# Kernel optimization log

Measured on AMD Instinct MI355X. Metric: run time of the kernel, lower is better.

Reference implementation:

```python
import jax, jax.numpy as jnp
import numpy as np

SEQ = 4096
D = 1024


def setup_inputs() -> dict:
    key = jax.random.key(0)
    kx, kq, kk, kv = jax.random.split(key, 4)
    x = jax.random.normal(kx, (SEQ, D), dtype=jnp.float32)
    W_Q = jax.random.normal(kq, (D, D), dtype=jnp.float32)
    W_K = jax.random.normal(kk, (D, D), dtype=jnp.float32)
    W_V = jax.random.normal(kv, (D, D), dtype=jnp.float32)
    b_Q = jnp.zeros((D,), dtype=jnp.float32)
    b_K = jnp.zeros((D,), dtype=jnp.float32)
    b_V = jnp.zeros((D,), dtype=jnp.float32)
    return {"x": x, "W_Q": W_Q, "W_K": W_K, "W_V": W_V,
            "b_Q": b_Q, "b_K": b_K, "b_V": b_V}


def reference(x, W_Q, W_K, W_V, b_Q, b_K, b_V):
    d_head = W_Q.shape[0]
    q = x @ W_Q + b_Q                      # [S, D]
    k = x @ W_K + b_K                      # [S, D]
    v = x @ W_V + b_V                      # [S, D]
    scores = (q @ k.T) / jnp.sqrt(jnp.float32(d_head))  # [S, S]
    probs = jax.nn.softmax(scores, axis=-1)              # softmax over last axis
    return probs @ v                        # [S, D]
```

## Files before the change

kernel.cpp:

```cpp
#include <hip/hip_runtime.h>
#include <hip/hip_bf16.h>
#include <stdint.h>

#define SEQLEN 4096
#define DMODEL 1024

typedef uint16_t u16;
typedef uint32_t u32;

typedef __bf16 bf16x8 __attribute__((ext_vector_type(8)));
typedef float  f32x4  __attribute__((ext_vector_type(4)));
typedef u16    u16x8  __attribute__((ext_vector_type(8)));
typedef u16    u16x4  __attribute__((ext_vector_type(4)));

__device__ __forceinline__ u16 f2bf(float f) {
  union { float f; u32 u; } a; a.f = f;
  return (u16)((a.u + 0x7FFFu + ((a.u >> 16) & 1u)) >> 16);
}
__device__ __forceinline__ float bf2f(u16 h) {
  union { u32 u; float f; } a; a.u = ((u32)h) << 16;
  return a.f;
}

__device__ __forceinline__ void gl_lds16(const u16* g, u16* l) {
  __builtin_amdgcn_global_load_lds(
      (const __attribute__((address_space(1))) void*)g,
      (__attribute__((address_space(3))) void*)l,
      16, 0, 0);
}

__device__ __forceinline__ void stage_tile(const u16* __restrict__ g, int ld,
                                           int row0, int k0, u16* lds, int tid) {
#pragma unroll
  for (int it = 0; it < 4; ++it) {
    int u = tid + 256 * it;
    int row = u >> 3;
    int cg = (u & 7) ^ (row & 7);
    gl_lds16(g + (size_t)(row0 + row) * ld + (size_t)(k0 + cg * 8), lds + u * 8);
  }
}

__device__ __forceinline__ bf16x8 ld_frag(const u16* lds, int row, int chunk) {
  return *(const bf16x8*)(lds + row * 64 + ((chunk ^ (row & 7)) << 3));
}

#define MFMA16(c, a, b) c = __builtin_amdgcn_mfma_f32_16x16x32_bf16(a, b, c, 0, 0, 0)

__global__ void split_x_kernel(const float* __restrict__ x,
                               u16* __restrict__ xh, u16* __restrict__ xl) {
  const int total = SEQLEN * DMODEL / 4;
  for (int idx = blockIdx.x * 256 + threadIdx.x; idx < total; idx += gridDim.x * 256) {
    float4 f = ((const float4*)x)[idx];
    float ff[4] = {f.x, f.y, f.z, f.w};
    union { u16x4 v; u16 s[4]; } h, l;
#pragma unroll
    for (int uu = 0; uu < 4; ++uu) {
      u16 hi = f2bf(ff[uu]);
      h.s[uu] = hi;
      l.s[uu] = f2bf(ff[uu] - bf2f(hi));
    }
    ((u16x4*)xh)[idx] = h.v;
    ((u16x4*)xl)[idx] = l.v;
  }
}

__global__ void transpose_w_kernel(const float* __restrict__ W,
                                   u16* __restrict__ wth, u16* __restrict__ wtl) {
  __shared__ float tile[64][65];
  int n0 = (blockIdx.x & 15) * 64;
  int k0 = (blockIdx.x >> 4) * 64;
  int c = threadIdx.x & 63, r0 = threadIdx.x >> 6;
#pragma unroll
  for (int rr = 0; rr < 16; ++rr) {
    int r = r0 * 16 + rr;
    tile[r][c] = W[(size_t)(k0 + r) * DMODEL + n0 + c];
  }
  __syncthreads();
#pragma unroll
  for (int rr = 0; rr < 16; ++rr) {
    int n = r0 * 16 + rr;
    float f = tile[c][n];
    u16 hi = f2bf(f);
    wth[(size_t)(n0 + n) * DMODEL + k0 + c] = hi;
    wtl[(size_t)(n0 + n) * DMODEL + k0 + c] = f2bf(f - bf2f(hi));
  }
}

template <bool THREE, bool SPLITOUT>
__global__ __launch_bounds__(256, 2) void proj_kernel(
    const u16* __restrict__ Ah, const u16* __restrict__ Al,
    const u16* __restrict__ Bh, const u16* __restrict__ Bl,
    const float* __restrict__ bias, float scale,
    u16* __restrict__ outh, u16* __restrict__ outl, u16* __restrict__ outT) {
  __shared__ __align__(16) u16 sAh[128 * 64];
  __shared__ __align__(16) u16 sBh[128 * 64];
  __shared__ __align__(16) u16 sAl[THREE ? 128 * 64 : 8];
  __shared__ __align__(16) u16 sBl[THREE ? 128 * 64 : 8];

  int tid = threadIdx.x;
  int lane = tid & 63, wid = tid >> 6;
  int wr = (wid >> 1) * 64, wc = (wid & 1) * 64;
  int r = lane & 15, g = lane >> 4;
  int m0 = blockIdx.x * 128, n0 = blockIdx.y * 128;

  f32x4 acc[4][4];
#pragma unroll
  for (int i = 0; i < 4; ++i)
#pragma unroll
    for (int j = 0; j < 4; ++j) acc[i][j] = (f32x4){0.f, 0.f, 0.f, 0.f};

  for (int step = 0; step < DMODEL / 64; ++step) {
    int k0 = step * 64;
    __syncthreads();
    stage_tile(Ah, DMODEL, m0, k0, sAh, tid);
    stage_tile(Bh, DMODEL, n0, k0, sBh, tid);
    if (THREE) {
      stage_tile(Al, DMODEL, m0, k0, sAl, tid);
      stage_tile(Bl, DMODEL, n0, k0, sBl, tid);
    }
    __syncthreads();
#pragma unroll
    for (int ks = 0; ks < 2; ++ks) {
      bf16x8 fa[4], fb[4], fal[4], fbl[4];
#pragma unroll
      for (int i = 0; i < 4; ++i) {
        fa[i] = ld_frag(sAh, wr + i * 16 + r, ks * 4 + g);
        fb[i] = ld_frag(sBh, wc + i * 16 + r, ks * 4 + g);
      }
      if (THREE) {
#pragma unroll
        for (int i = 0; i < 4; ++i) {
          fal[i] = ld_frag(sAl, wr + i * 16 + r, ks * 4 + g);
          fbl[i] = ld_frag(sBl, wc + i * 16 + r, ks * 4 + g);
        }
      }
#pragma unroll
      for (int i = 0; i < 4; ++i)
#pragma unroll
        for (int j = 0; j < 4; ++j) {
          MFMA16(acc[i][j], fa[i], fb[j]);
          if (THREE) {
            MFMA16(acc[i][j], fa[i], fbl[j]);
            MFMA16(acc[i][j], fal[i], fb[j]);
          }
        }
    }
  }
#pragma unroll
  for (int i = 0; i < 4; ++i)
#pragma unroll
    for (int j = 0; j < 4; ++j) {
      int col = n0 + wc + j * 16 + r;
      float bv = bias[col];
#pragma unroll
      for (int t = 0; t < 4; ++t) {
        int row = m0 + wr + i * 16 + g * 4 + t;
        float v = (acc[i][j][t] + bv) * scale;
        if (SPLITOUT) {
          u16 hi = f2bf(v);
          outh[(size_t)row * DMODEL + col] = hi;
          outl[(size_t)row * DMODEL + col] = f2bf(v - bf2f(hi));
        } else {
          outT[(size_t)col * SEQLEN + row] = f2bf(v);
        }
      }
    }
}

__global__ __launch_bounds__(256, 2) void scores_kernel(
    const u16* __restrict__ qh, const u16* __restrict__ ql,
    const u16* __restrict__ kh, const u16* __restrict__ kl,
    u16* __restrict__ P, float* __restrict__ mloc, float* __restrict__ tsum) {
  __shared__ __align__(16) float sS[128 * 129];
  u16* sAh = (u16*)sS;
  u16* sAl = sAh + 128 * 64;
  u16* sBh = sAl + 128 * 64;
  u16* sBl = sBh + 128 * 64;

  int tid = threadIdx.x;
  int lane = tid & 63, wid = tid >> 6;
  int wr = (wid >> 1) * 64, wc = (wid & 1) * 64;
  int r = lane & 15, g = lane >> 4;
  int m0 = blockIdx.x * 128, n0 = blockIdx.y * 128;

  f32x4 acc[4][4];
#pragma unroll
  for (int i = 0; i < 4; ++i)
#pragma unroll
    for (int j = 0; j < 4; ++j) acc[i][j] = (f32x4){0.f, 0.f, 0.f, 0.f};

  for (int step = 0; step < DMODEL / 64; ++step) {
    int k0 = step * 64;
    __syncthreads();
    stage_tile(qh, DMODEL, m0, k0, sAh, tid);
    stage_tile(kh, DMODEL, n0, k0, sBh, tid);
    stage_tile(ql, DMODEL, m0, k0, sAl, tid);
    stage_tile(kl, DMODEL, n0, k0, sBl, tid);
    __syncthreads();
#pragma unroll
    for (int ks = 0; ks < 2; ++ks) {
      bf16x8 fa[4], fb[4], fal[4], fbl[4];
#pragma unroll
      for (int i = 0; i < 4; ++i) {
        fa[i] = ld_frag(sAh, wr + i * 16 + r, ks * 4 + g);
        fb[i] = ld_frag(sBh, wc + i * 16 + r, ks * 4 + g);
        fal[i] = ld_frag(sAl, wr + i * 16 + r, ks * 4 + g);
        fbl[i] = ld_frag(sBl, wc + i * 16 + r, ks * 4 + g);
      }
#pragma unroll
      for (int i = 0; i < 4; ++i)
#pragma unroll
        for (int j = 0; j < 4; ++j) {
          MFMA16(acc[i][j], fa[i], fb[j]);
          MFMA16(acc[i][j], fa[i], fbl[j]);
          MFMA16(acc[i][j], fal[i], fb[j]);
        }
    }
  }
  __syncthreads();
#pragma unroll
  for (int i = 0; i < 4; ++i)
#pragma unroll
    for (int j = 0; j < 4; ++j)
#pragma unroll
      for (int t = 0; t < 4; ++t)
        sS[(wr + i * 16 + g * 4 + t) * 129 + wc + j * 16 + r] = acc[i][j][t];
  __syncthreads();

  int rt = tid >> 1, h = tid & 1;
  const float* rowp = sS + rt * 129 + h * 64;
  float mx = -3.0e38f;
#pragma unroll 16
  for (int c = 0; c < 64; ++c) mx = fmaxf(mx, rowp[c]);
  mx = fmaxf(mx, __shfl_xor(mx, 1));

  float ssum = 0.f;
  int grow = m0 + rt;
  u16* pout = P + (size_t)grow * SEQLEN + n0 + h * 64;
#pragma unroll
  for (int c8 = 0; c8 < 8; ++c8) {
    union { u16 s[8]; u16x8 v; } tmp;
#pragma unroll
    for (int uu = 0; uu < 8; ++uu) {
      float e = exp2f((rowp[c8 * 8 + uu] - mx) * 1.4426950408889634f);
      ssum += e;
      tmp.s[uu] = f2bf(e);
    }
    *(u16x8*)(pout + c8 * 8) = tmp.v;
  }
  ssum += __shfl_xor(ssum, 1);
  if (h == 0) {
    mloc[(size_t)blockIdx.y * SEQLEN + grow] = mx;
    tsum[(size_t)blockIdx.y * SEQLEN + grow] = ssum;
  }
}

__global__ void finalize_kernel(const float* __restrict__ mloc,
                                const float* __restrict__ tsum,
                                float* __restrict__ rowscale) {
  int rr = blockIdx.x * 256 + threadIdx.x;
  if (rr >= SEQLEN) return;
  float M = -3.0e38f;
#pragma unroll
  for (int t = 0; t < 32; ++t) M = fmaxf(M, mloc[t * SEQLEN + rr]);
  float l = 0.f;
#pragma unroll
  for (int t = 0; t < 32; ++t)
    l += tsum[t * SEQLEN + rr] * exp2f((mloc[t * SEQLEN + rr] - M) * 1.4426950408889634f);
  float inv = 1.0f / l;
#pragma unroll
  for (int t = 0; t < 32; ++t)
    rowscale[t * SEQLEN + rr] = exp2f((mloc[t * SEQLEN + rr] - M) * 1.4426950408889634f) * inv;
}

__global__ void pnorm_kernel(u16* __restrict__ P, const float* __restrict__ rowscale) {
  const int total = SEQLEN * SEQLEN / 8;
  for (int idx = blockIdx.x * 256 + threadIdx.x; idx < total; idx += gridDim.x * 256) {
    int rrow = idx >> 9;
    int c8 = idx & 511;
    int t = c8 >> 4;
    float sc = rowscale[t * SEQLEN + rrow];
    union { u16x8 v; u16 s[8]; } d;
    d.v = ((u16x8*)P)[idx];
#pragma unroll
    for (int uu = 0; uu < 8; ++uu) d.s[uu] = f2bf(bf2f(d.s[uu]) * sc);
    ((u16x8*)P)[idx] = d.v;
  }
}

__global__ __launch_bounds__(256, 2) void pv_kernel(const u16* __restrict__ P,
                                                    const u16* __restrict__ vT,
                                                    float* __restrict__ out) {
  __shared__ __align__(16) u16 sA[128 * 64];
  __shared__ __align__(16) u16 sB[128 * 64];
  int tid = threadIdx.x;
  int lane = tid & 63, wid = tid >> 6;
  int wr = (wid >> 1) * 64, wc = (wid & 1) * 64;
  int r = lane & 15, g = lane >> 4;
  int m0 = blockIdx.x * 128, n0 = blockIdx.y * 128;

  f32x4 acc[4][4];
#pragma unroll
  for (int i = 0; i < 4; ++i)
#pragma unroll
    for (int j = 0; j < 4; ++j) acc[i][j] = (f32x4){0.f, 0.f, 0.f, 0.f};

  for (int step = 0; step < SEQLEN / 64; ++step) {
    int k0 = step * 64;
    __syncthreads();
    stage_tile(P, SEQLEN, m0, k0, sA, tid);
    stage_tile(vT, SEQLEN, n0, k0, sB, tid);
    __syncthreads();
#pragma unroll
    for (int ks = 0; ks < 2; ++ks) {
      bf16x8 fa[4], fb[4];
#pragma unroll
      for (int i = 0; i < 4; ++i) {
        fa[i] = ld_frag(sA, wr + i * 16 + r, ks * 4 + g);
        fb[i] = ld_frag(sB, wc + i * 16 + r, ks * 4 + g);
      }
#pragma unroll
      for (int i = 0; i < 4; ++i)
#pragma unroll
        for (int j = 0; j < 4; ++j) MFMA16(acc[i][j], fa[i], fb[j]);
    }
  }
#pragma unroll
  for (int i = 0; i < 4; ++i)
#pragma unroll
    for (int j = 0; j < 4; ++j)
#pragma unroll
      for (int t = 0; t < 4; ++t)
        out[(size_t)(m0 + wr + i * 16 + g * 4 + t) * DMODEL + n0 + wc + j * 16 + r] =
            acc[i][j][t];
}

extern "C" void kernel_launch(void* const* d_in, const int* in_sizes, int n_in,
                              void* d_out, int out_size, void* d_ws, size_t ws_size,
                              hipStream_t stream) {
  (void)in_sizes; (void)n_in; (void)out_size; (void)ws_size;
  const float* x  = (const float*)d_in[0];
  const float* WQ = (const float*)d_in[1];
  const float* WK = (const float*)d_in[2];
  const float* WV = (const float*)d_in[3];
  const float* bQ = (const float*)d_in[4];
  const float* bK = (const float*)d_in[5];
  const float* bV = (const float*)d_in[6];
  float* out = (float*)d_out;
  char* ws = (char*)d_ws;
  const size_t MB = 1ull << 20;

  u16* xh   = (u16*)(ws + 0);
  u16* xl   = (u16*)(ws + 8 * MB);
  u16* wqh  = (u16*)(ws + 16 * MB);
  u16* wql  = (u16*)(ws + 18 * MB);
  u16* wkh  = (u16*)(ws + 20 * MB);
  u16* wkl  = (u16*)(ws + 22 * MB);
  u16* wvh  = (u16*)(ws + 24 * MB);
  u16* wvl  = (u16*)(ws + 26 * MB);
  u16* P    = (u16*)(ws + 0);
  u16* qh   = (u16*)(ws + 32 * MB);
  u16* ql   = (u16*)(ws + 40 * MB);
  u16* kh   = (u16*)(ws + 48 * MB);
  u16* kl   = (u16*)(ws + 56 * MB);
  u16* vT   = (u16*)(ws + 64 * MB);
  float* mloc     = (float*)(ws + 72 * MB);
  float* tsum     = (float*)(ws + 72 * MB + 512 * 1024);
  float* rowscale = (float*)(ws + 73 * MB);

  split_x_kernel<<<2048, 256, 0, stream>>>(x, xh, xl);
  transpose_w_kernel<<<256, 256, 0, stream>>>(WQ, wqh, wql);
  transpose_w_kernel<<<256, 256, 0, stream>>>(WK, wkh, wkl);
  transpose_w_kernel<<<256, 256, 0, stream>>>(WV, wvh, wvl);

  dim3 gproj(32, 8);
  proj_kernel<true, true><<<gproj, 256, 0, stream>>>(xh, xl, wqh, wql, bQ,
                                                     1.0f / 32.0f, qh, ql, nullptr);
  proj_kernel<true, true><<<gproj, 256, 0, stream>>>(xh, xl, wkh, wkl, bK,
                                                     1.0f, kh, kl, nullptr);
  proj_kernel<false, false><<<gproj, 256, 0, stream>>>(xh, nullptr, wvh, nullptr, bV,
                                                       1.0f, nullptr, nullptr, vT);

  dim3 gsc(32, 32);
  scores_kernel<<<gsc, 256, 0, stream>>>(qh, ql, kh, kl, P, mloc, tsum);
  finalize_kernel<<<16, 256, 0, stream>>>(mloc, tsum, rowscale);
  pnorm_kernel<<<4096, 256, 0, stream>>>(P, rowscale);

  dim3 gpv(32, 8);
  pv_kernel<<<gpv, 256, 0, stream>>>(P, vT, out);
}
```

Before: 341.4 us.

## Double-buffer LDS staging in projection, scores and PV GEMM kernels

Converts the GEMM main loops to a double-buffered LDS scheme. The next K-tile is prefetched with global_load_lds while the current tile feeds the MFMAs, so there is one barrier per step instead of two. The three-pass split-bf16 kernels halve the K-step to 32 with a new swizzle, keeping LDS at 64KB. This aims to hide global load latency behind compute. The costs are more LDS per block, which may limit occupancy, and a possible race because the async loads are not explicitly waited on before the barrier.

```diff
diff --git a/kernel.cpp b/kernel.cpp
--- a/kernel.cpp
+++ b/kernel.cpp
@@ -29,8 +29,8 @@
       16, 0, 0);
 }
 
-__device__ __forceinline__ void stage_tile(const u16* __restrict__ g, int ld,
-                                           int row0, int k0, u16* lds, int tid) {
+__device__ __forceinline__ void stage64(const u16* __restrict__ g, int ld,
+                                        int row0, int k0, u16* lds, int tid) {
 #pragma unroll
   for (int it = 0; it < 4; ++it) {
     int u = tid + 256 * it;
@@ -39,9 +39,21 @@
     gl_lds16(g + (size_t)(row0 + row) * ld + (size_t)(k0 + cg * 8), lds + u * 8);
   }
 }
-
-__device__ __forceinline__ bf16x8 ld_frag(const u16* lds, int row, int chunk) {
+__device__ __forceinline__ void stage32(const u16* __restrict__ g, int ld,
+                                        int row0, int k0, u16* lds, int tid) {
+#pragma unroll
+  for (int it = 0; it < 2; ++it) {
+    int u = tid + 256 * it;
+    int row = u >> 2;
+    int cg = (u & 3) ^ ((row >> 1) & 3);
+    gl_lds16(g + (size_t)(row0 + row) * ld + (size_t)(k0 + cg * 8), lds + u * 8);
+  }
+}
+__device__ __forceinline__ bf16x8 frag64(const u16* lds, int row, int chunk) {
   return *(const bf16x8*)(lds + row * 64 + ((chunk ^ (row & 7)) << 3));
+}
+__device__ __forceinline__ bf16x8 frag32(const u16* lds, int row, int chunk) {
+  return *(const bf16x8*)(lds + row * 32 + ((chunk ^ ((row >> 1) & 3)) << 3));
 }
 
 #define MFMA16(c, a, b) c = __builtin_amdgcn_mfma_f32_16x16x32_bf16(a, b, c, 0, 0, 0)
@@ -92,10 +104,7 @@
     const u16* __restrict__ Bh, const u16* __restrict__ Bl,
     const float* __restrict__ bias, float scale,
     u16* __restrict__ outh, u16* __restrict__ outl, u16* __restrict__ outT) {
-  __shared__ __align__(16) u16 sAh[128 * 64];
-  __shared__ __align__(16) u16 sBh[128 * 64];
-  __shared__ __align__(16) u16 sAl[THREE ? 128 * 64 : 8];
-  __shared__ __align__(16) u16 sBl[THREE ? 128 * 64 : 8];
+  __shared__ __align__(16) u16 st[32768];
 
   int tid = threadIdx.x;
   int lane = tid & 63, wid = tid >> 6;
@@ -109,43 +118,73 @@
 #pragma unroll
     for (int j = 0; j < 4; ++j) acc[i][j] = (f32x4){0.f, 0.f, 0.f, 0.f};
 
-  for (int step = 0; step < DMODEL / 64; ++step) {
-    int k0 = step * 64;
+  if (THREE) {
+    stage32(Ah, DMODEL, m0, 0, st + 0 * 4096, tid);
+    stage32(Al, DMODEL, m0, 0, st + 1 * 4096, tid);
+    stage32(Bh, DMODEL, n0, 0, st + 2 * 4096, tid);
+    stage32(Bl, DMODEL, n0, 0, st + 3 * 4096, tid);
     __syncthreads();
-    stage_tile(Ah, DMODEL, m0, k0, sAh, tid);
-    stage_tile(Bh, DMODEL, n0, k0, sBh, tid);
-    if (THREE) {
-      stage_tile(Al, DMODEL, m0, k0, sAl, tid);
-      stage_tile(Bl, DMODEL, n0, k0, sBl, tid);
-    }
-    __syncthreads();
-#pragma unroll
-    for (int ks = 0; ks < 2; ++ks) {
+    int c = 0;
+    for (int step = 0; step < DMODEL / 32; ++step) {
+      if (step + 1 < DMODEL / 32) {
+        int k0 = (step + 1) * 32;
+        u16* nb = st + (c ^ 1) * 16384;
+        stage32(Ah, DMODEL, m0, k0, nb + 0 * 4096, tid);
+        stage32(Al, DMODEL, m0, k0, nb + 1 * 4096, tid);
+        stage32(Bh, DMODEL, n0, k0, nb + 2 * 4096, tid);
+        stage32(Bl, DMODEL, n0, k0, nb + 3 * 4096, tid);
+      }
+      const u16* cb = st + c * 16384;
       bf16x8 fa[4], fb[4], fal[4], fbl[4];
 #pragma unroll
       for (int i = 0; i < 4; ++i) {
-        fa[i] = ld_frag(sAh, wr + i * 16 + r, ks * 4 + g);
-        fb[i] = ld_frag(sBh, wc + i * 16 + r, ks * 4 + g);
-      }
-      if (THREE) {
-#pragma unroll
-        for (int i = 0; i < 4; ++i) {
-          fal[i] = ld_frag(sAl, wr + i * 16 + r, ks * 4 + g);
-          fbl[i] = ld_frag(sBl, wc + i * 16 + r, ks * 4 + g);
-        }
+        fa[i]  = frag32(cb + 0 * 4096, wr + i * 16 + r, g);
+        fal[i] = frag32(cb + 1 * 4096, wr + i * 16 + r, g);
+        fb[i]  = frag32(cb + 2 * 4096, wc + i * 16 + r, g);
+        fbl[i] = frag32(cb + 3 * 4096, wc + i * 16 + r, g);
       }
 #pragma unroll
       for (int i = 0; i < 4; ++i)
 #pragma unroll
         for (int j = 0; j < 4; ++j) {
           MFMA16(acc[i][j], fa[i], fb[j]);
-          if (THREE) {
-            MFMA16(acc[i][j], fa[i], fbl[j]);
-            MFMA16(acc[i][j], fal[i], fb[j]);
-          }
+          MFMA16(acc[i][j], fa[i], fbl[j]);
+          MFMA16(acc[i][j], fal[i], fb[j]);
         }
-    }
-  }
+      __syncthreads();
+      c ^= 1;
+    }
+  } else {
+    stage64(Ah, DMODEL, m0, 0, st + 0 * 8192, tid);
+    stage64(Bh, DMODEL, n0, 0, st + 1 * 8192, tid);
+    __syncthreads();
+    int c = 0;
+    for (int step = 0; step < DMODEL / 64; ++step) {
+      if (step + 1 < DMODEL / 64) {
+        int k0 = (step + 1) * 64;
+        u16* nb = st + (c ^ 1) * 16384;
+        stage64(Ah, DMODEL, m0, k0, nb + 0 * 8192, tid);
+        stage64(Bh, DMODEL, n0, k0, nb + 1 * 8192, tid);
+      }
+      const u16* cb = st + c * 16384;
+#pragma unroll
+      for (int ks = 0; ks < 2; ++ks) {
+        bf16x8 fa[4], fb[4];
+#pragma unroll
+        for (int i = 0; i < 4; ++i) {
+          fa[i] = frag64(cb + 0 * 8192, wr + i * 16 + r, ks * 4 + g);
+          fb[i] = frag64(cb + 1 * 8192, wc + i * 16 + r, ks * 4 + g);
+        }
+#pragma unroll
+        for (int i = 0; i < 4; ++i)
+#pragma unroll
+          for (int j = 0; j < 4; ++j) MFMA16(acc[i][j], fa[i], fb[j]);
+      }
+      __syncthreads();
+      c ^= 1;
+    }
+  }
+
 #pragma unroll
   for (int i = 0; i < 4; ++i)
 #pragma unroll
@@ -171,11 +210,9 @@
     const u16* __restrict__ qh, const u16* __restrict__ ql,
     const u16* __restrict__ kh, const u16* __restrict__ kl,
     u16* __restrict__ P, float* __restrict__ mloc, float* __restrict__ tsum) {
-  __shared__ __align__(16) float sS[128 * 129];
-  u16* sAh = (u16*)sS;
-  u16* sAl = sAh + 128 * 64;
-  u16* sBh = sAl + 128 * 64;
-  u16* sBl = sBh + 128 * 64;
+  __shared__ __align__(16) char smem[128 * 129 * 4];
+  u16* st = (u16*)smem;
+  float* sS = (float*)smem;
 
   int tid = threadIdx.x;
   int lane = tid & 63, wid = tid >> 6;
@@ -189,35 +226,42 @@
 #pragma unroll
     for (int j = 0; j < 4; ++j) acc[i][j] = (f32x4){0.f, 0.f, 0.f, 0.f};
 
-  for (int step = 0; step < DMODEL / 64; ++step) {
-    int k0 = step * 64;
+  stage32(qh, DMODEL, m0, 0, st + 0 * 4096, tid);
+  stage32(ql, DMODEL, m0, 0, st + 1 * 4096, tid);
+  stage32(kh, DMODEL, n0, 0, st + 2 * 4096, tid);
+  stage32(kl, DMODEL, n0, 0, st + 3 * 4096, tid);
+  __syncthreads();
+  int c = 0;
+  for (int step = 0; step < DMODEL / 32; ++step) {
+    if (step + 1 < DMODEL / 32) {
+      int k0 = (step + 1) * 32;
+      u16* nb = st + (c ^ 1) * 16384;
+      stage32(qh, DMODEL, m0, k0, nb + 0 * 4096, tid);
+      stage32(ql, DMODEL, m0, k0, nb + 1 * 4096, tid);
+      stage32(kh, DMODEL, n0, k0, nb + 2 * 4096, tid);
+      stage32(kl, DMODEL, n0, k0, nb + 3 * 4096, tid);
+    }
+    const u16* cb = st + c * 16384;
+    bf16x8 fa[4], fb[4], fal[4], fbl[4];
+#pragma unroll
+    for (int i = 0; i < 4; ++i) {
+      fa[i]  = frag32(cb + 0 * 4096, wr + i * 16 + r, g);
+      fal[i] = frag32(cb + 1 * 4096, wr + i * 16 + r, g);
+      fb[i]  = frag32(cb + 2 * 4096, wc + i * 16 + r, g);
+      fbl[i] = frag32(cb + 3 * 4096, wc + i * 16 + r, g);
+    }
+#pragma unroll
+    for (int i = 0; i < 4; ++i)
+#pragma unroll
+      for (int j = 0; j < 4; ++j) {
+        MFMA16(acc[i][j], fa[i], fb[j]);
+        MFMA16(acc[i][j], fa[i], fbl[j]);
+        MFMA16(acc[i][j], fal[i], fb[j]);
+      }
     __syncthreads();
-    stage_tile(qh, DMODEL, m0, k0, sAh, tid);
-    stage_tile(kh, DMODEL, n0, k0, sBh, tid);
-    stage_tile(ql, DMODEL, m0, k0, sAl, tid);
-    stage_tile(kl, DMODEL, n0, k0, sBl, tid);
-    __syncthreads();
-#pragma unroll
-    for (int ks = 0; ks < 2; ++ks) {
-      bf16x8 fa[4], fb[4], fal[4], fbl[4];
-#pragma unroll
-      for (int i = 0; i < 4; ++i) {
-        fa[i] = ld_frag(sAh, wr + i * 16 + r, ks * 4 + g);
-        fb[i] = ld_frag(sBh, wc + i * 16 + r, ks * 4 + g);
-        fal[i] = ld_frag(sAl, wr + i * 16 + r, ks * 4 + g);
-        fbl[i] = ld_frag(sBl, wc + i * 16 + r, ks * 4 + g);
-      }
-#pragma unroll
-      for (int i = 0; i < 4; ++i)
-#pragma unroll
-        for (int j = 0; j < 4; ++j) {
-          MFMA16(acc[i][j], fa[i], fb[j]);
-          MFMA16(acc[i][j], fa[i], fbl[j]);
-          MFMA16(acc[i][j], fal[i], fb[j]);
-        }
-    }
-  }
-  __syncthreads();
+    c ^= 1;
+  }
+
 #pragma unroll
   for (int i = 0; i < 4; ++i)
 #pragma unroll
@@ -231,7 +275,7 @@
   const float* rowp = sS + rt * 129 + h * 64;
   float mx = -3.0e38f;
 #pragma unroll 16
-  for (int c = 0; c < 64; ++c) mx = fmaxf(mx, rowp[c]);
+  for (int cc = 0; cc < 64; ++cc) mx = fmaxf(mx, rowp[cc]);
   mx = fmaxf(mx, __shfl_xor(mx, 1));
 
   float ssum = 0.f;
@@ -291,8 +335,7 @@
 __global__ __launch_bounds__(256, 2) void pv_kernel(const u16* __restrict__ P,
                                                     const u16* __restrict__ vT,
                                                     float* __restrict__ out) {
-  __shared__ __align__(16) u16 sA[128 * 64];
-  __shared__ __align__(16) u16 sB[128 * 64];
+  __shared__ __align__(16) u16 st[32768];
   int tid = threadIdx.x;
   int lane = tid & 63, wid = tid >> 6;
   int wr = (wid >> 1) * 64, wc = (wid & 1) * 64;
@@ -305,25 +348,33 @@
 #pragma unroll
     for (int j = 0; j < 4; ++j) acc[i][j] = (f32x4){0.f, 0.f, 0.f, 0.f};
 
+  stage64(P, SEQLEN, m0, 0, st + 0 * 8192, tid);
+  stage64(vT, SEQLEN, n0, 0, st + 1 * 8192, tid);
+  __syncthreads();
+  int c = 0;
   for (int step = 0; step < SEQLEN / 64; ++step) {
-    int k0 = step * 64;
-    __syncthreads();
-    stage_tile(P, SEQLEN, m0, k0, sA, tid);
-    stage_tile(vT, SEQLEN, n0, k0, sB, tid);
-    __syncthreads();
+    if (step + 1 < SEQLEN / 64) {
+      int k0 = (step + 1) * 64;
+      u16* nb = st + (c ^ 1) * 16384;
+      stage64(P, SEQLEN, m0, k0, nb + 0 * 8192, tid);
+      stage64(vT, SEQLEN, n0, k0, nb + 1 * 8192, tid);
+    }
+    const u16* cb = st + c * 16384;
 #pragma unroll
     for (int ks = 0; ks < 2; ++ks) {
       bf16x8 fa[4], fb[4];
 #pragma unroll
       for (int i = 0; i < 4; ++i) {
-        fa[i] = ld_frag(sA, wr + i * 16 + r, ks * 4 + g);
-        fb[i] = ld_frag(sB, wc + i * 16 + r, ks * 4 + g);
+        fa[i] = frag64(cb + 0 * 8192, wr + i * 16 + r, ks * 4 + g);
+        fb[i] = frag64(cb + 1 * 8192, wc + i * 16 + r, ks * 4 + g);
       }
 #pragma unroll
       for (int i = 0; i < 4; ++i)
 #pragma unroll
         for (int j = 0; j < 4; ++j) MFMA16(acc[i][j], fa[i], fb[j]);
     }
+    __syncthreads();
+    c ^= 1;
   }
 #pragma unroll
   for (int i = 0; i < 4; ++i)
```

After: 337.8 us. About the same (-1.1%).
